# Kernel optimization log

Measured on AMD Instinct MI355X. Metric: run time of the kernel, lower is better.

## Reference

```python
import jax, jax.numpy as jnp
import numpy as np

B, C, H, W = 4, 64, 128, 128
CQ = C // 8
EPS = 1e-5


def setup_inputs() -> dict:
    key = jax.random.key(0)
    ks = jax.random.split(key, 20)
    r = lambda k, shape, s=0.05: jax.random.normal(k, shape, dtype=jnp.float32) * s
    return {
        "x1": jax.random.normal(ks[0], (B, C, H, W), dtype=jnp.float32),
        "x2": jax.random.normal(ks[1], (B, C, H, W), dtype=jnp.float32),
        # 1x1 convs are plain channel matmuls: weight (out, in), bias (out,)
        "wqA": r(ks[2], (CQ, C)), "bqA": r(ks[3], (CQ,)),
        "wkA": r(ks[4], (CQ, C)), "bkA": r(ks[5], (CQ,)),
        "wvA": r(ks[6], (C, C)),  "bvA": r(ks[7], (C,)),
        "wqB": r(ks[8], (CQ, C)), "bqB": r(ks[9], (CQ,)),
        "wkB": r(ks[10], (CQ, C)), "bkB": r(ks[11], (CQ,)),
        "wvB": r(ks[12], (C, C)),  "bvB": r(ks[13], (C,)),
        "gA": r(ks[14], (1,), 0.1), "gB": r(ks[15], (1,), 0.1),
        "wp": r(ks[16], (C, C)), "bp": r(ks[17], (C,)),
        "bn_g": jnp.ones((C,), dtype=jnp.float32),
        "bn_b": jnp.zeros((C,), dtype=jnp.float32),
    }


def _conv1(x, w, b):
    # 1x1 conv over NCHW == per-pixel channel matmul
    return jnp.einsum('oi,bihw->bohw', w, x) + b[None, :, None, None]


def _axial(q, k, v):
    # criss-cross attention: for each pixel, attend over its row and column,
    # with the column (H) self-position masked to -inf, joint softmax over H+W.
    h = q.shape[2]
    eH = jnp.einsum('bciw,bcjw->biwj', q, k)            # [B,H,W,H] column scores
    eH = jnp.where(jnp.eye(h, dtype=bool)[:, None, :], -jnp.inf, eH)
    eW = jnp.einsum('bchi,bchj->bhij', q, k)            # [B,H,W,W] row scores
    att = jax.nn.softmax(jnp.concatenate([eH, eW], axis=3), axis=3)
    oH = jnp.einsum('bcjw,biwj->bciw', v, att[..., :h])
    oW = jnp.einsum('bchj,bhij->bchi', v, att[..., h:])
    return oH + oW


def _forward(x1, x2, wqA, bqA, wkA, bkA, wvA, bvA, wqB, bqB, wkB, bkB, wvB, bvB,
             gA, gB, wp, bp, bn_g, bn_b):
    # branch A: query from x2, key/value from x1
    out_A = _axial(_conv1(x2, wqA, bqA), _conv1(x1, wkA, bkA), _conv1(x1, wvA, bvA))
    # branch B: query/key/value all from x1
    out_B = _axial(_conv1(x1, wqB, bqB), _conv1(x1, wkB, bkB), _conv1(x1, wvB, bvB))
    diff = jnp.abs(out_A - out_B)
    p = jax.nn.gelu(_conv1(diff, wp, bp), approximate=False)
    # BatchNorm2d in training mode: batch statistics, biased variance
    m = p.mean(axis=(0, 2, 3), keepdims=True)
    v = ((p - m) ** 2).mean(axis=(0, 2, 3), keepdims=True)
    out = (p - m) / jnp.sqrt(v + EPS) * bn_g[None, :, None, None] + bn_b[None, :, None, None]
    return gA[0] * out_A + x1 + out, gB[0] * out_B + x2 + out


def reference(x1, x2, wqA, bqA, wkA, bkA, wvA, bvA, wqB, bqB, wkB, bkB, wvB, bvB,
              gA, gB, wp, bp, bn_g, bn_b):
    return _forward(x1, x2, wqA, bqA, wkA, bkA, wvA, bvA, wqB, bqB, wkB, bkB,
                    wvB, bvB, gA, gB, wp, bp, bn_g, bn_b)
```

## Files before the change

### kernel.cpp

```cpp
#include <hip/hip_runtime.h>


#define NE 4194304ull

typedef __attribute__((ext_vector_type(8))) short short8;
typedef __attribute__((ext_vector_type(4))) float f32x4;

#define HD __device__ __forceinline__

HD float b2f(unsigned short u) { union { unsigned int i; float f; } v; v.i = ((unsigned int)u) << 16; return v.f; }
HD unsigned short f2b(float x) {
  union { float f; unsigned int i; } v; v.f = x;
  unsigned int r = v.i + 0x7FFFu + ((v.i >> 16) & 1u);
  return (unsigned short)(r >> 16);
}

HD void up8(uint4 u, float* o) {
  o[0] = b2f((unsigned short)(u.x & 0xffff)); o[1] = b2f((unsigned short)(u.x >> 16));
  o[2] = b2f((unsigned short)(u.y & 0xffff)); o[3] = b2f((unsigned short)(u.y >> 16));
  o[4] = b2f((unsigned short)(u.z & 0xffff)); o[5] = b2f((unsigned short)(u.z >> 16));
  o[6] = b2f((unsigned short)(u.w & 0xffff)); o[7] = b2f((unsigned short)(u.w >> 16));
}

HD float dot8(const float* q, uint4 u) {
  float s;
  s  = q[0]*b2f((unsigned short)(u.x & 0xffff)) + q[1]*b2f((unsigned short)(u.x >> 16));
  s += q[2]*b2f((unsigned short)(u.y & 0xffff)) + q[3]*b2f((unsigned short)(u.y >> 16));
  s += q[4]*b2f((unsigned short)(u.z & 0xffff)) + q[5]*b2f((unsigned short)(u.z >> 16));
  s += q[6]*b2f((unsigned short)(u.w & 0xffff)) + q[7]*b2f((unsigned short)(u.w >> 16));
  return s;
}

HD float erf_fast(float x) {
  const float ax = fabsf(x);
  const float t = 1.0f / (1.0f + 0.3275911f * ax);
  const float poly = ((((1.061405429f*t - 1.453152027f)*t + 1.421413741f)*t
                       - 0.284496736f)*t + 0.254829592f)*t;
  const float y = 1.0f - poly * __expf(-ax*ax);
  return copysignf(y, x);
}

HD unsigned short ldbf(const void* s0, int i, int f) {
  return f ? f2b(((const float*)s0)[i]) : ((const unsigned short*)s0)[i];
}

__global__ __launch_bounds__(256) void prelude_kernel(
    const void* x1,
    const void* wqA, const void* bqA, const void* wkA, const void* bkA,
    const void* wvA, const void* bvA, const void* wqB, const void* bqB,
    const void* wkB, const void* bkB, const void* wvB, const void* bvB,
    const void* wp, const void* bp, const void* gA, const void* gB,
    const void* bng, const void* bnb,
    int* flag, unsigned short* wout)
{
  __shared__ int s;
  if (threadIdx.x == 0) s = 0;
  __syncthreads();
  const float a = fabsf(b2f(((const unsigned short*)x1)[threadIdx.x]));
  if (a > 1000.0f) atomicOr(&s, 1);
  __syncthreads();
  const int f = s;
  if (blockIdx.x == 0 && threadIdx.x == 0) *flag = f;

  const void* srcs[18] = {wqA,bqA,wkA,bkA,wvA,bvA,wqB,bqB,wkB,bkB,wvB,bvB,wp,bp,gA,gB,bng,bnb};
  const int   ns[18]   = {512,  8,512,  8,4096, 64,512,  8,512,  8,4096, 64,4096,64, 1, 1, 64, 64};
  unsigned short* wqkv = wout + 14696;
  float* wbias = (float*)(wout + 25960);

  const int gstride = gridDim.x * 256;
  for (int idx = blockIdx.x*256 + threadIdx.x; idx < 26136; idx += gstride) {
    if (idx < 14690) {
      int off = idx, k2 = 0;
      while (off >= ns[k2]) { off -= ns[k2]; ++k2; }
      wout[idx] = ldbf(srcs[k2], off, f);
    } else if (idx >= 25960) {
      const int i3 = idx - 25960, mt = i3 >> 4, r = i3 & 15;
      float val = 0.0f;
      if (mt == 0)      { if (r < 8) val = b2f(ldbf(bqA, r, f)); }
      else if (mt == 1) { val = b2f((r < 8) ? ldbf(bkA, r, f) : ldbf(bqB, r - 8, f)); }
      else if (mt == 2) { if (r < 8) val = b2f(ldbf(bkB, r, f)); }
      else if (mt < 7)  { val = b2f(ldbf(bvA, (mt-3)*16 + r, f)); }
      else              { val = b2f(ldbf(bvB, (mt-7)*16 + r, f)); }
      wbias[i3] = val;
    } else if (idx >= 14696) {
      const int i2 = idx - 14696;
      const int mt = i2 >> 10, rem = i2 & 1023, r = rem >> 6, ci = rem & 63;
      unsigned short val = 0;
      if (mt == 0)      { if (r < 8) val = ldbf(wqA, r*64 + ci, f); }
      else if (mt == 1) { val = (r < 8) ? ldbf(wkA, r*64 + ci, f) : ldbf(wqB, (r-8)*64 + ci, f); }
      else if (mt == 2) { if (r < 8) val = ldbf(wkB, r*64 + ci, f); }
      else if (mt < 7)  { val = ldbf(wvA, ((mt-3)*16 + r)*64 + ci, f); }
      else              { val = ldbf(wvB, ((mt-7)*16 + r)*64 + ci, f); }
      wqkv[i2] = val;
    }
  }
}

__global__ __launch_bounds__(256) void qkv_kernel(
    const void* __restrict__ x1v, const void* __restrict__ x2v, const int* __restrict__ flag,
    const unsigned short* __restrict__ wqkv, const float* __restrict__ wbias,
    unsigned short* __restrict__ q, unsigned short* __restrict__ k,
    unsigned short* __restrict__ v)
{
  const int hp = blockIdx.x, b = blockIdx.y;
  const int h0 = hp*2;
  const int tid = threadIdx.x, lane = tid & 63, w4 = tid >> 6;
  const int col = lane & 15, quad = lane >> 4;
  const int f32m = *flag;
  __shared__ __align__(16) char smem[33792];
  unsigned short* Xb = (unsigned short*)smem;
  unsigned short* S0 = (unsigned short*)smem;
  unsigned short* S1 = (unsigned short*)(smem + 8448);
  const size_t gb = (size_t)b*1048576 + (size_t)h0*128;

  short8 Bc[2][8];
  #pragma unroll
  for (int pass = 0; pass < 2; ++pass) {
    const void* xv = pass ? x2v : x1v;
    for (int t = tid; t < 2048; t += 256) {
      const int c = t >> 5, rem = t & 31, hh = rem >> 4, w8 = (rem & 15)*8;
      const int n = hh*128 + w8;
      const size_t a = gb + (size_t)c*16384 + (size_t)hh*128 + w8;
      unsigned short vals[8];
      if (f32m) {
        const float* xf = (const float*)xv;
        const float4 f0 = *(const float4*)(xf + a);
        const float4 f1 = *(const float4*)(xf + a + 4);
        vals[0]=f2b(f0.x); vals[1]=f2b(f0.y); vals[2]=f2b(f0.z); vals[3]=f2b(f0.w);
        vals[4]=f2b(f1.x); vals[5]=f2b(f1.y); vals[6]=f2b(f1.z); vals[7]=f2b(f1.w);
      } else {
        const uint4 u = *(const uint4*)((const unsigned short*)xv + a);
        vals[0]=(unsigned short)(u.x & 0xffff); vals[1]=(unsigned short)(u.x >> 16);
        vals[2]=(unsigned short)(u.y & 0xffff); vals[3]=(unsigned short)(u.y >> 16);
        vals[4]=(unsigned short)(u.z & 0xffff); vals[5]=(unsigned short)(u.z >> 16);
        vals[6]=(unsigned short)(u.w & 0xffff); vals[7]=(unsigned short)(u.w >> 16);
      }
      #pragma unroll
      for (int i = 0; i < 8; ++i) Xb[(n + i)*66 + c] = vals[i];
    }
    __syncthreads();
    const unsigned int* U = (const unsigned int*)Xb;
    #pragma unroll
    for (int nt = 0; nt < 4; ++nt)
      #pragma unroll
      for (int ks = 0; ks < 2; ++ks) {
        const int n = w4*64 + nt*16 + col;
        const int base = n*33 + (ks*32 + quad*8)/2;
        union { unsigned int u32[4]; short8 s; } p;
        #pragma unroll
        for (int jj = 0; jj < 4; ++jj) p.u32[jj] = U[base + jj];
        Bc[pass][nt*2 + ks] = p.s;
      }
    __syncthreads();
  }

  #pragma unroll
  for (int mt = 0; mt < 11; ++mt) {
    f32x4 acc[4];
    #pragma unroll
    for (int nt = 0; nt < 4; ++nt) acc[nt] = (f32x4){0.f, 0.f, 0.f, 0.f};
    #pragma unroll
    for (int ks = 0; ks < 2; ++ks) {
      union { uint4 u; short8 s; } A;
      A.u = *(const uint4*)(wqkv + mt*1024 + col*64 + ks*32 + quad*8);
      #pragma unroll
      for (int nt = 0; nt < 4; ++nt)
        acc[nt] = __builtin_amdgcn_mfma_f32_16x16x32_bf16(
            A.s, (mt == 0) ? Bc[1][nt*2 + ks] : Bc[0][nt*2 + ks], acc[nt], 0, 0, 0);
    }
    float bias[4];
    #pragma unroll
    for (int r = 0; r < 4; ++r) bias[r] = wbias[mt*16 + quad*4 + r];
    unsigned short* S = (mt & 1) ? S1 : S0;
    #pragma unroll
    for (int nt = 0; nt < 4; ++nt)
      #pragma unroll
      for (int r = 0; r < 4; ++r) {
        const int row = quad*4 + r;
        const int nloc = w4*64 + nt*16 + col;
        S[row*264 + nloc] = f2b(acc[nt][r] + bias[r]);
      }
    __syncthreads();
    if (mt < 3) {
      const int nloc = tid;
      const int pixg = h0*128 + nloc;
      union { unsigned short u[8]; uint4 v4; } P;
      #pragma unroll
      for (int r = 0; r < 8; ++r) P.u[r] = S[r*264 + nloc];
      if (mt == 0) {
        *(uint4*)(q + ((size_t)b*16384 + pixg)*8) = P.v4;
      } else if (mt == 1) {
        *(uint4*)(k + ((size_t)b*16384 + pixg)*8) = P.v4;
        #pragma unroll
        for (int r = 0; r < 8; ++r) P.u[r] = S[(8 + r)*264 + nloc];
        *(uint4*)(q + ((size_t)(4 + b)*16384 + pixg)*8) = P.v4;
      } else {
        *(uint4*)(k + ((size_t)(4 + b)*16384 + pixg)*8) = P.v4;
      }
    } else {
      const int vm = (mt >= 7) ? mt - 7 : mt - 3;
      const int z  = (mt >= 7) ? 4 + b : b;
      const int cl = tid >> 4, u = tid & 15;
      const int co = vm*16 + cl;
      const uint4 a0 = *(const uint4*)&S[cl*264 + u*16];
      const uint4 a1 = *(const uint4*)&S[cl*264 + u*16 + 8];
      unsigned short* dst = v + ((size_t)(z*64 + co)*16384 + (size_t)h0*128 + u*16);
      *(uint4*)dst = a0;
      *(uint4*)(dst + 8) = a1;
    }
  }
}

__global__ __launch_bounds__(256) void transpose_v(
    const unsigned short* __restrict__ vStd, unsigned short* __restrict__ vT)
{
  const int tile = blockIdx.x, c = blockIdx.y, z = blockIdx.z;
  const int h0 = (tile & 3) * 32, w0 = (tile >> 2) * 32;
  const size_t base = ((size_t)z*64 + c) * 16384;
  __shared__ unsigned short T[32][33];
  const int tid = threadIdx.x;
  for (int idx = tid; idx < 1024; idx += 256) {
    const int r = idx >> 5, cc = idx & 31;
    T[r][cc] = vStd[base + (size_t)(h0 + r)*128 + (w0 + cc)];
  }
  __syncthreads();
  for (int idx = tid; idx < 1024; idx += 256) {
    const int r = idx >> 5, cc = idx & 31;
    vT[base + (size_t)(w0 + r)*128 + (h0 + cc)] = T[cc][r];
  }
}

__global__ __launch_bounds__(256) void pv_kernel(
    const unsigned short* __restrict__ q, const unsigned short* __restrict__ k,
    const unsigned short* __restrict__ vStd, const unsigned short* __restrict__ vT,
    float* __restrict__ outBrF, float* __restrict__ oColF,
    float* __restrict__ lRow, float* __restrict__ lCol)
{
  const int X = blockIdx.x, b = blockIdx.y;
  const int br = blockIdx.z & 1, dir = blockIdx.z >> 1;
  const int tid = threadIdx.x, lane = tid & 63, w4 = tid >> 6;
  const int z = br*4 + b;
  const size_t b4h = (size_t)z * 128;
  __shared__ uint4 Ks[128];
  __shared__ __align__(16) char smem[34048];
  uint4* Vl = (uint4*)smem;
  float* Dst = (float*)smem;

  if (tid < 128) {
    const int j = tid;
    const size_t pix = (b4h + (dir ? X : j))*128 + (dir ? j : X);
    Ks[j] = *(const uint4*)(k + pix*8);
  }
  const unsigned short* vsrc = dir ? vStd : vT;
  const size_t vbase = ((size_t)z*64)*16384 + (size_t)X*128;
  for (int t = tid; t < 1024; t += 256) {
    const int vl = t & 63, nb = (t >> 6) & 3, kb = t >> 8;
    const int c = nb*16 + (vl & 15), j0 = kb*32 + ((vl >> 4) << 3);
    Vl[t] = *(const uint4*)(vsrc + vbase + (size_t)c*16384 + j0);
  }
  __syncthreads();

  float* lOut = dir ? lRow : lCol;
  short8 af[2][4];
  #pragma unroll
  for (int ib2 = 0; ib2 < 2; ++ib2) {
    const int ib = w4*2 + ib2;
    const int m = ib*16 + (lane & 15);
    const size_t pix = (b4h + (dir ? X : m))*128 + (dir ? m : X);
    float qv[8]; up8(*(const uint4*)(q + pix*8), qv);
    float lsum = 0.0f;
    #pragma unroll
    for (int kb = 0; kb < 4; ++kb) {
      const int jbase = kb*32 + ((lane >> 4) << 3);
      union { unsigned short u[8]; short8 s; } pk;
      #pragma unroll
      for (int jj = 0; jj < 8; ++jj) {
        const int j = jbase + jj;
        float p = 0.0f;
        if (dir || (j != m)) p = __expf(dot8(qv, Ks[j]));
        lsum += p;
        pk.u[jj] = f2b(p);
      }
      af[ib2][kb] = pk.s;
    }
    lsum += __shfl_xor(lsum, 16);
    lsum += __shfl_xor(lsum, 32);
    if (lane < 16) lOut[((size_t)z*128 + X)*128 + ib*16 + lane] = lsum;
  }

  f32x4 acc[2][4];
  #pragma unroll
  for (int i2 = 0; i2 < 2; ++i2)
    #pragma unroll
    for (int nb = 0; nb < 4; ++nb) acc[i2][nb] = (f32x4){0.f, 0.f, 0.f, 0.f};
  #pragma unroll
  for (int nb = 0; nb < 4; ++nb)
    #pragma unroll
    for (int kb = 0; kb < 4; ++kb) {
      const short8 bfr = *(short8*)&Vl[(kb*4 + nb)*64 + lane];
      acc[0][nb] = __builtin_amdgcn_mfma_f32_16x16x32_bf16(af[0][kb], bfr, acc[0][nb], 0, 0, 0);
      acc[1][nb] = __builtin_amdgcn_mfma_f32_16x16x32_bf16(af[1][kb], bfr, acc[1][nb], 0, 0, 0);
    }
  __syncthreads();

  #pragma unroll
  for (int i2 = 0; i2 < 2; ++i2)
    #pragma unroll
    for (int nb = 0; nb < 4; ++nb)
      #pragma unroll
      for (int r = 0; r < 4; ++r) {
        const int mm = (w4*2 + i2)*16 + ((lane >> 4) << 2) + r;
        const int cc = nb*16 + (lane & 15);
        Dst[cc*133 + mm] = acc[i2][nb][r];
      }
  __syncthreads();
  float* dst = dir ? outBrF : oColF;
  for (int t = tid; t < 8192; t += 256) {
    const int cc = t >> 7, mm = t & 127;
    dst[vbase + (size_t)cc*16384 + mm] = Dst[cc*133 + mm];
  }
}

__global__ __launch_bounds__(256) void combine_kernel(
    const float* __restrict__ oColU, const float* __restrict__ lRow,
    const float* __restrict__ lCol, float* __restrict__ outBr)
{
  const int tile = blockIdx.x, z = blockIdx.y, cg = blockIdx.z;
  const int h0 = (tile & 3) * 32, w0 = (tile >> 2) * 32, c0 = cg*8;
  const int tid = threadIdx.x;
  __shared__ float Tl[32][33];
  __shared__ __align__(16) float inv[32][36];
  __shared__ __align__(16) float T4[4][32][36];
  const size_t lzb = (size_t)z * 16384;
  {
    const int w = tid >> 3, h4 = (tid & 7)*4;
    const float4 vc = *(const float4*)(lCol + lzb + (size_t)(w0 + w)*128 + h0 + h4);
    Tl[w][h4+0] = vc.x; Tl[w][h4+1] = vc.y; Tl[w][h4+2] = vc.z; Tl[w][h4+3] = vc.w;
  }
  __syncthreads();
  {
    const int h = tid >> 3, w4 = (tid & 7)*4;
    const float4 lr = *(const float4*)(lRow + lzb + (size_t)(h0 + h)*128 + w0 + w4);
    float4 iv;
    iv.x = 1.0f / (lr.x + Tl[w4+0][h]);
    iv.y = 1.0f / (lr.y + Tl[w4+1][h]);
    iv.z = 1.0f / (lr.z + Tl[w4+2][h]);
    iv.w = 1.0f / (lr.w + Tl[w4+3][h]);
    *(float4*)&inv[h][w4] = iv;
  }
  __syncthreads();
  #pragma unroll
  for (int half = 0; half < 2; ++half) {
    for (int t = tid; t < 1024; t += 256) {
      const int ch = t >> 8, rem = t & 255, w = rem >> 3, h4 = (rem & 7)*4;
      const int c = c0 + half*4 + ch;
      const float4 vc = *(const float4*)(oColU + ((size_t)(z*64 + c))*16384
                                         + (size_t)(w0 + w)*128 + h0 + h4);
      *(float4*)&T4[ch][w][h4] = vc;
    }
    __syncthreads();
    for (int t = tid; t < 1024; t += 256) {
      const int ch = t >> 8, rem = t & 255, h = rem >> 3, w4 = (rem & 7)*4;
      const int c = c0 + half*4 + ch;
      const size_t off = ((size_t)(z*64 + c))*16384 + (size_t)(h0 + h)*128 + w0 + w4;
      float4 o = *(const float4*)(outBr + off);
      const float4 iv = *(const float4*)&inv[h][w4];
      o.x = (o.x + T4[ch][w4+0][h]) * iv.x;
      o.y = (o.y + T4[ch][w4+1][h]) * iv.y;
      o.z = (o.z + T4[ch][w4+2][h]) * iv.z;
      o.w = (o.w + T4[ch][w4+3][h]) * iv.w;
      *(float4*)(outBr + off) = o;
    }
    __syncthreads();
  }
}

__global__ __launch_bounds__(256) void proj_kernel(
    const float* __restrict__ outA, const float* __restrict__ outB,
    const unsigned short* __restrict__ wp, const unsigned short* __restrict__ bp,
    float* __restrict__ pbuf, float* __restrict__ part)
{
  const int h = blockIdx.x, b = blockIdx.y, wh = blockIdx.z, tid = threadIdx.x;
  const int blk = ((h*4 + b)*2 + wh);
  __shared__ __align__(16) float diffs[64][64];
  for (int idx = tid; idx < 4096; idx += 256) {
    const int c = idx >> 6, w = idx & 63;
    const size_t off = ((size_t)(b*64 + c)*128 + h)*128 + wh*64 + w;
    diffs[c][w] = fabsf(outA[off] - outB[off]);
  }
  __syncthreads();
  const int cog = tid >> 5, wl = tid & 31;
  float acc[8][2];
  #pragma unroll
  for (int c8 = 0; c8 < 8; ++c8) { acc[c8][0] = 0.f; acc[c8][1] = 0.f; }
  for (int cb = 0; cb < 8; ++cb) {
    uint4 wrow[8];
    #pragma unroll
    for (int c8 = 0; c8 < 8; ++c8) wrow[c8] = *(const uint4*)&wp[(cog*8 + c8)*64 + cb*8];
    #pragma unroll
    for (int t = 0; t < 8; ++t) {
      const int ci = cb*8 + t;
      const float d0 = diffs[ci][wl], d1 = diffs[ci][wl + 32];
      #pragma unroll
      for (int c8 = 0; c8 < 8; ++c8) {
        const float wf = b2f(((const unsigned short*)&wrow[c8])[t]);
        acc[c8][0] += wf*d0; acc[c8][1] += wf*d1;
      }
    }
  }
  #pragma unroll
  for (int c8 = 0; c8 < 8; ++c8) {
    const int co = cog*8 + c8;
    const float bias = b2f(bp[co]);
    const size_t pb = ((size_t)(b*64 + co)*128 + h)*128 + wh*64;
    float s1 = 0.f, s2 = 0.f;
    #pragma unroll
    for (int t = 0; t < 2; ++t) {
      const float x = acc[c8][t] + bias;
      const float g = 0.5f * x * (1.0f + erf_fast(x * 0.70710678118f));
      pbuf[pb + wl + t*32] = g;
      s1 += g; s2 += g*g;
    }
    #pragma unroll
    for (int off = 16; off >= 1; off >>= 1) { s1 += __shfl_xor(s1, off); s2 += __shfl_xor(s2, off); }
    if (wl == 0) {
      part[(size_t)co*1024 + blk] = s1;
      part[(size_t)(64 + co)*1024 + blk] = s2;
    }
  }
}

__global__ __launch_bounds__(256) void reduce_kernel(
    const float* __restrict__ part, float* __restrict__ bnAcc)
{
  const int stat = blockIdx.x, tid = threadIdx.x;
  const float4 v = *(const float4*)(part + (size_t)stat*1024 + tid*4);
  float s = v.x + v.y + v.z + v.w;
  #pragma unroll
  for (int off = 32; off >= 1; off >>= 1) s += __shfl_xor(s, off);
  __shared__ float ws4[4];
  if ((tid & 63) == 0) ws4[tid >> 6] = s;
  __syncthreads();
  if (tid == 0) bnAcc[stat] = ws4[0] + ws4[1] + ws4[2] + ws4[3];
}

__global__ __launch_bounds__(256) void final_kernel(
    const float* __restrict__ pbuf, const float* __restrict__ outA, const float* __restrict__ outB,
    const void* __restrict__ x1v, const void* __restrict__ x2v, const int* __restrict__ flag,
    const unsigned short* __restrict__ gA, const unsigned short* __restrict__ gB,
    const unsigned short* __restrict__ bng, const unsigned short* __restrict__ bnb,
    const float* __restrict__ bnAcc, void* __restrict__ outv)
{
  const int f32m = *flag;
  const int idx = (blockIdx.x * 256 + threadIdx.x) * 4;
  const int c = (idx >> 14) & 63;
  const float invN = 1.0f / 65536.0f;
  const float s1 = bnAcc[c], s2 = bnAcc[64 + c];
  const float mean = s1 * invN;
  const float var = s2 * invN - mean*mean;
  const float scale = rsqrtf(var + 1e-5f) * b2f(bng[c]);
  const float beta = b2f(bnb[c]);
  const float ga = b2f(gA[0]), gb = b2f(gB[0]);
  const float4 p4 = *(const float4*)(pbuf + idx);
  const float4 a4 = *(const float4*)(outA + idx);
  const float4 b4 = *(const float4*)(outB + idx);
  float p[4] = {p4.x, p4.y, p4.z, p4.w};
  float a[4] = {a4.x, a4.y, a4.z, a4.w};
  float bb[4] = {b4.x, b4.y, b4.z, b4.w};
  float xa[4], xb[4];
  if (f32m) {
    const float4 t1 = *(const float4*)((const float*)x1v + idx);
    const float4 t2 = *(const float4*)((const float*)x2v + idx);
    xa[0]=t1.x; xa[1]=t1.y; xa[2]=t1.z; xa[3]=t1.w;
    xb[0]=t2.x; xb[1]=t2.y; xb[2]=t2.z; xb[3]=t2.w;
  } else {
    const uint2 x1u = *(const uint2*)((const unsigned short*)x1v + idx);
    const uint2 x2u = *(const uint2*)((const unsigned short*)x2v + idx);
    xa[0] = b2f((unsigned short)(x1u.x & 0xffff)); xa[1] = b2f((unsigned short)(x1u.x >> 16));
    xa[2] = b2f((unsigned short)(x1u.y & 0xffff)); xa[3] = b2f((unsigned short)(x1u.y >> 16));
    xb[0] = b2f((unsigned short)(x2u.x & 0xffff)); xb[1] = b2f((unsigned short)(x2u.x >> 16));
    xb[2] = b2f((unsigned short)(x2u.y & 0xffff)); xb[3] = b2f((unsigned short)(x2u.y >> 16));
  }
  float o1f[4], o2f[4];
  #pragma unroll
  for (int t = 0; t < 4; ++t) {
    const float nv = (p[t] - mean)*scale + beta;
    o1f[t] = ga*a[t] + xa[t] + nv;
    o2f[t] = gb*bb[t] + xb[t] + nv;
  }
  if (f32m) {
    float* of = (float*)outv;
    *(float4*)(of + idx)      = (float4){o1f[0], o1f[1], o1f[2], o1f[3]};
    *(float4*)(of + NE + idx) = (float4){o2f[0], o2f[1], o2f[2], o2f[3]};
  } else {
    unsigned short* oh = (unsigned short*)outv;
    uint2 u1, u2;
    u1.x = (unsigned int)f2b(o1f[0]) | ((unsigned int)f2b(o1f[1]) << 16);
    u1.y = (unsigned int)f2b(o1f[2]) | ((unsigned int)f2b(o1f[3]) << 16);
    u2.x = (unsigned int)f2b(o2f[0]) | ((unsigned int)f2b(o2f[1]) << 16);
    u2.y = (unsigned int)f2b(o2f[2]) | ((unsigned int)f2b(o2f[3]) << 16);
    *(uint2*)(oh + idx) = u1;
    *(uint2*)(oh + NE + idx) = u2;
  }
}

extern "C" void kernel_launch(void* const* d_in, const int* in_sizes, int n_in,
                              void* d_out, int out_size, void* d_ws, size_t ws_size,
                              hipStream_t stream)
{
  const void* x1  = d_in[0];
  const void* x2  = d_in[1];

  char* ws = (char*)d_ws;
  const size_t MB = 1048576ull;
  unsigned short* q     = (unsigned short*)(ws);
  unsigned short* kk    = (unsigned short*)(ws + 2*MB);
  float* lRow           = (float*)(ws + 4*MB);
  float* lCol           = (float*)(ws + 4*MB + 512*1024);
  unsigned short* vStd  = (unsigned short*)(ws + 6*MB);
  unsigned short* vT    = (unsigned short*)(ws + 22*MB);
  float* outBr          = (float*)(ws + 38*MB);
  float* oColF          = (float*)(ws + 70*MB);
  float* pbuf           = (float*)(ws + 70*MB);
  float* part           = (float*)(ws + 86*MB);
  float* bnAcc          = (float*)(ws + 102*MB);
  int*   flag           = (int*)(ws + 102*MB + 512);
  unsigned short* wC    = (unsigned short*)(ws + 102*MB + 1024);

  prelude_kernel<<<64, 256, 0, stream>>>(
      x1, d_in[2], d_in[3], d_in[4], d_in[5], d_in[6], d_in[7], d_in[8], d_in[9],
      d_in[10], d_in[11], d_in[12], d_in[13], d_in[16], d_in[17], d_in[14], d_in[15],
      d_in[18], d_in[19], flag, wC);
  qkv_kernel<<<dim3(64, 4), 256, 0, stream>>>(
      x1, x2, flag, wC + 14696, (const float*)(wC + 25960), q, kk, vStd);
  transpose_v<<<dim3(16, 64, 8), 256, 0, stream>>>(vStd, vT);
  pv_kernel<<<dim3(128, 4, 4), 256, 0, stream>>>(q, kk, vStd, vT, outBr, oColF, lRow, lCol);
  combine_kernel<<<dim3(16, 8, 8), 256, 0, stream>>>(oColF, lRow, lCol, outBr);
  proj_kernel<<<dim3(128, 4, 2), 256, 0, stream>>>(outBr, outBr + NE, wC + 10400, wC + 14496, pbuf, part);
  reduce_kernel<<<128, 256, 0, stream>>>(part, bnAcc);
  final_kernel<<<4096, 256, 0, stream>>>(pbuf, outBr, outBr + NE, x1, x2, flag,
                                         wC + 14560, wC + 14561, wC + 14562, wC + 14626,
                                         bnAcc, d_out);
}
```

Measured before the change: 243.4 us.

## Compute Q·K attention scores with MFMA and stage probabilities through LDS

The 8-channel query-key dot products in pv_kernel were computed with scalar FMAs per thread and unpacked from bf16. They now run as zero-padded 16x16x32 bf16 MFMAs; the exponentiated probabilities are written to a shared-memory P tile and read back in the A-fragment layout for the PV MFMA. K and V now share one LDS buffer, which adds an extra barrier and an LDS round trip for P. The 8-channel K dimension is padded to 32, so three quarters of each score MFMA does no useful work.

```diff
diff --git a/kernel.cpp b/kernel.cpp
--- a/kernel.cpp
+++ b/kernel.cpp
@@ -13,22 +13,6 @@
   union { float f; unsigned int i; } v; v.f = x;
   unsigned int r = v.i + 0x7FFFu + ((v.i >> 16) & 1u);
   return (unsigned short)(r >> 16);
-}
-
-HD void up8(uint4 u, float* o) {
-  o[0] = b2f((unsigned short)(u.x & 0xffff)); o[1] = b2f((unsigned short)(u.x >> 16));
-  o[2] = b2f((unsigned short)(u.y & 0xffff)); o[3] = b2f((unsigned short)(u.y >> 16));
-  o[4] = b2f((unsigned short)(u.z & 0xffff)); o[5] = b2f((unsigned short)(u.z >> 16));
-  o[6] = b2f((unsigned short)(u.w & 0xffff)); o[7] = b2f((unsigned short)(u.w >> 16));
-}
-
-HD float dot8(const float* q, uint4 u) {
-  float s;
-  s  = q[0]*b2f((unsigned short)(u.x & 0xffff)) + q[1]*b2f((unsigned short)(u.x >> 16));
-  s += q[2]*b2f((unsigned short)(u.y & 0xffff)) + q[3]*b2f((unsigned short)(u.y >> 16));
-  s += q[4]*b2f((unsigned short)(u.z & 0xffff)) + q[5]*b2f((unsigned short)(u.z >> 16));
-  s += q[6]*b2f((unsigned short)(u.w & 0xffff)) + q[7]*b2f((unsigned short)(u.w >> 16));
-  return s;
 }
 
 HD float erf_fast(float x) {
@@ -239,17 +223,88 @@
   const int X = blockIdx.x, b = blockIdx.y;
   const int br = blockIdx.z & 1, dir = blockIdx.z >> 1;
   const int tid = threadIdx.x, lane = tid & 63, w4 = tid >> 6;
+  const int col = lane & 15, quad = lane >> 4;
   const int z = br*4 + b;
   const size_t b4h = (size_t)z * 128;
-  __shared__ uint4 Ks[128];
-  __shared__ __align__(16) char smem[34048];
-  uint4* Vl = (uint4*)smem;
-  float* Dst = (float*)smem;
+  __shared__ __align__(16) char smemA[34048];
+  __shared__ __align__(16) char smemB[16384];
+  unsigned short* P = (unsigned short*)smemA;
+  float* Dst = (float*)smemA;
+  uint4* Ks = (uint4*)smemB;
+  uint4* Vl = (uint4*)smemB;
 
   if (tid < 128) {
     const int j = tid;
     const size_t pix = (b4h + (dir ? X : j))*128 + (dir ? j : X);
     Ks[j] = *(const uint4*)(k + pix*8);
+  }
+  __syncthreads();
+
+  const uint4 zero4 = {0u, 0u, 0u, 0u};
+  short8 Afr[2];
+  #pragma unroll
+  for (int ib2 = 0; ib2 < 2; ++ib2) {
+    uint4 a = zero4;
+    if (quad == 0) {
+      const int m = (w4*2 + ib2)*16 + col;
+      const size_t pix = (b4h + (dir ? X : m))*128 + (dir ? m : X);
+      a = *(const uint4*)(q + pix*8);
+    }
+    union { uint4 u; short8 s; } cv; cv.u = a; Afr[ib2] = cv.s;
+  }
+  float lsum[2][4];
+  #pragma unroll
+  for (int ib2 = 0; ib2 < 2; ++ib2)
+    #pragma unroll
+    for (int r = 0; r < 4; ++r) lsum[ib2][r] = 0.0f;
+  #pragma unroll
+  for (int nb = 0; nb < 8; ++nb) {
+    uint4 bu = (quad == 0) ? Ks[nb*16 + col] : zero4;
+    union { uint4 u; short8 s; } bv; bv.u = bu;
+    f32x4 sA = __builtin_amdgcn_mfma_f32_16x16x32_bf16(Afr[0], bv.s, (f32x4){0.f,0.f,0.f,0.f}, 0, 0, 0);
+    f32x4 sB = __builtin_amdgcn_mfma_f32_16x16x32_bf16(Afr[1], bv.s, (f32x4){0.f,0.f,0.f,0.f}, 0, 0, 0);
+    const int j = nb*16 + col;
+    #pragma unroll
+    for (int ib2 = 0; ib2 < 2; ++ib2) {
+      const int mbase = (w4*2 + ib2)*16 + quad*4;
+      #pragma unroll
+      for (int r = 0; r < 4; ++r) {
+        const int m = mbase + r;
+        const float sv = ib2 ? sB[r] : sA[r];
+        float p = 0.0f;
+        if (dir || (j != m)) p = __expf(sv);
+        lsum[ib2][r] += p;
+        P[m*132 + j] = f2b(p);
+      }
+    }
+  }
+  #pragma unroll
+  for (int ib2 = 0; ib2 < 2; ++ib2)
+    #pragma unroll
+    for (int r = 0; r < 4; ++r) {
+      float s = lsum[ib2][r];
+      s += __shfl_xor(s, 1); s += __shfl_xor(s, 2);
+      s += __shfl_xor(s, 4); s += __shfl_xor(s, 8);
+      if (col == 0) {
+        const int m = (w4*2 + ib2)*16 + quad*4 + r;
+        float* lOut = dir ? lRow : lCol;
+        lOut[((size_t)z*128 + X)*128 + m] = s;
+      }
+    }
+  __syncthreads();
+
+  short8 af[2][4];
+  #pragma unroll
+  for (int ib2 = 0; ib2 < 2; ++ib2) {
+    const int m = (w4*2 + ib2)*16 + col;
+    #pragma unroll
+    for (int kb = 0; kb < 4; ++kb) {
+      const int j0 = kb*32 + quad*8;
+      union { uint2 u[2]; short8 s; } pk;
+      pk.u[0] = *(const uint2*)&P[m*132 + j0];
+      pk.u[1] = *(const uint2*)&P[m*132 + j0 + 4];
+      af[ib2][kb] = pk.s;
+    }
   }
   const unsigned short* vsrc = dir ? vStd : vT;
   const size_t vbase = ((size_t)z*64)*16384 + (size_t)X*128;
@@ -259,34 +314,6 @@
     Vl[t] = *(const uint4*)(vsrc + vbase + (size_t)c*16384 + j0);
   }
   __syncthreads();
-
-  float* lOut = dir ? lRow : lCol;
-  short8 af[2][4];
-  #pragma unroll
-  for (int ib2 = 0; ib2 < 2; ++ib2) {
-    const int ib = w4*2 + ib2;
-    const int m = ib*16 + (lane & 15);
-    const size_t pix = (b4h + (dir ? X : m))*128 + (dir ? m : X);
-    float qv[8]; up8(*(const uint4*)(q + pix*8), qv);
-    float lsum = 0.0f;
-    #pragma unroll
-    for (int kb = 0; kb < 4; ++kb) {
-      const int jbase = kb*32 + ((lane >> 4) << 3);
-      union { unsigned short u[8]; short8 s; } pk;
-      #pragma unroll
-      for (int jj = 0; jj < 8; ++jj) {
-        const int j = jbase + jj;
-        float p = 0.0f;
-        if (dir || (j != m)) p = __expf(dot8(qv, Ks[j]));
-        lsum += p;
-        pk.u[jj] = f2b(p);
-      }
-      af[ib2][kb] = pk.s;
-    }
-    lsum += __shfl_xor(lsum, 16);
-    lsum += __shfl_xor(lsum, 32);
-    if (lane < 16) lOut[((size_t)z*128 + X)*128 + ib*16 + lane] = lsum;
-  }
 
   f32x4 acc[2][4];
   #pragma unroll
```

New measurement: 234.7 us. 1.04x faster.
